# Optimization experiments

Hardware: AMD Instinct MI355X
Metric: run time of the kernel (lower is better)

Reference implementation:

```python
import jax, jax.numpy as jnp
import numpy as np

B, T, C = 8, 2048, 512
H = 16
HS = C // H  # 32, must equal HEAD_SIZE
TM_DIM = 32   # TIME_MIX_EXTRA_DIM
TD_DIM = 64   # TIME_DECAY_EXTRA_DIM
LAYER_ID, N_LAYER = 5, 12


def setup_inputs() -> dict:
    key = jax.random.key(0)
    ks = jax.random.split(key, 16)
    r01 = LAYER_ID / (N_LAYER - 1)
    r1a0 = 1.0 - LAYER_ID / N_LAYER
    ddd = (jnp.arange(C, dtype=jnp.float32) / C)
    n = jnp.arange(C, dtype=jnp.float32)
    decay_speed = -6.0 + 5.0 * (n / (C - 1)) ** (0.7 + 1.3 * r01)
    zigzag = ((n + 1) % 3 - 1) * 0.1
    faaaa = (r01 * (1 - n / (C - 1)) + zigzag).reshape(H, HS)
    s = 1.0 / np.sqrt(C)
    return {
        "x": jax.random.normal(ks[0], (B, T, C), dtype=jnp.float32),
        "time_maa_x": 1.0 - ddd ** r1a0,
        "time_maa_w": 1.0 - ddd ** r1a0,
        "time_maa_k": 1.0 - ddd ** r1a0,
        "time_maa_v": 1.0 - (ddd ** r1a0 + 0.3 * r01),
        "time_maa_r": 1.0 - ddd ** (0.5 * r1a0),
        "time_maa_g": 1.0 - ddd ** (0.5 * r1a0),
        "time_maa_w1": jax.random.uniform(ks[1], (C, TM_DIM * 5), minval=-1e-4, maxval=1e-4),
        "time_maa_w2": jax.random.uniform(ks[2], (5, TM_DIM, C), minval=-1e-4, maxval=1e-4),
        "time_decay": decay_speed,
        "time_decay_w1": jax.random.uniform(ks[3], (C, TD_DIM), minval=-1e-4, maxval=1e-4),
        "time_decay_w2": jax.random.uniform(ks[4], (TD_DIM, C), minval=-1e-4, maxval=1e-4),
        "time_faaaa": faaaa,
        "Wr": jax.random.normal(ks[5], (C, C)) * s,
        "Wk": jax.random.normal(ks[6], (C, C)) * s,
        "Wv": jax.random.normal(ks[7], (C, C)) * s,
        "Wg": jax.random.normal(ks[8], (C, C)) * s,
        "Wo": jax.random.normal(ks[9], (C, C)) * s,
        "ln_w": jnp.ones((C,), dtype=jnp.float32),
        "ln_b": jnp.zeros((C,), dtype=jnp.float32),
    }


def _wkv6(r, k, v, w, u):
    # r,k,v,w: (B,T,C); u: (H,HS). Linear recurrence per (batch, head).
    rs = r.reshape(B, T, H, HS).transpose(1, 0, 2, 3)
    ks_ = k.reshape(B, T, H, HS).transpose(1, 0, 2, 3)
    vs = v.reshape(B, T, H, HS).transpose(1, 0, 2, 3)
    # decay = exp(-exp(w)) per channel (the kernel passes ew = -exp(w))
    ds = jnp.exp(-jnp.exp(w.astype(jnp.float32))).reshape(B, T, H, HS).transpose(1, 0, 2, 3)
    ub = u[None, :, :, None]  # (1,H,HS_key,1)

    def step(S, inp):  # S: (B,H,HS_key,HS_val)
        r_t, k_t, v_t, d_t = inp
        kv = jnp.einsum("bhj,bhi->bhji", k_t, v_t)
        y = jnp.einsum("bhj,bhji->bhi", r_t, S + ub * kv)
        S = d_t[..., None] * S + kv
        return S, y

    S0 = jnp.zeros((B, H, HS, HS), dtype=jnp.float32)
    _, ys = jax.lax.scan(step, S0, (rs, ks_, vs, ds))
    return ys.transpose(1, 0, 2, 3).reshape(B, T, C)


def reference(x, time_maa_x, time_maa_w, time_maa_k, time_maa_v, time_maa_r,
              time_maa_g, time_maa_w1, time_maa_w2, time_decay, time_decay_w1,
              time_decay_w2, time_faaaa, Wr, Wk, Wv, Wg, Wo, ln_w, ln_b):
    # time shift: x_{t-1}, zeros at t=0  (ZeroPad2d((0,0,1,-1)))
    xshift = jnp.concatenate([jnp.zeros_like(x[:, :1]), x[:, :-1]], axis=1)
    xx = xshift - x
    xxx = x + xx * time_maa_x
    mix = jnp.tanh(jnp.einsum("btc,cd->btd", xxx, time_maa_w1)).reshape(B, T, 5, TM_DIM)
    mix = jnp.einsum("btfd,fdc->fbtc", mix, time_maa_w2)  # (5,B,T,C)
    mw, mk, mv, mr, mg = mix[0], mix[1], mix[2], mix[3], mix[4]
    xw = x + xx * (time_maa_w + mw)
    xk = x + xx * (time_maa_k + mk)
    xv = x + xx * (time_maa_v + mv)
    xr = x + xx * (time_maa_r + mr)
    xg = x + xx * (time_maa_g + mg)
    r = xr @ Wr.T
    k = xk @ Wk.T
    v = xv @ Wv.T
    g = jax.nn.silu(xg @ Wg.T)
    w = time_decay + jnp.tanh(xw @ time_decay_w1) @ time_decay_w2
    y = _wkv6(r, k, v, w, time_faaaa)
    # GroupNorm with H groups over channel dim, eps=1e-5
    yg = y.reshape(B, T, H, HS)
    mu = yg.mean(-1, keepdims=True)
    var = yg.var(-1, keepdims=True)
    yn = ((yg - mu) * jax.lax.rsqrt(var + 1e-5)).reshape(B, T, C)
    yn = yn * ln_w + ln_b
    return (yn * g) @ Wo.T
```

## Files before the change

kernel.cpp:

```cpp
#include <hip/hip_runtime.h>
#include <hip/hip_bf16.h>

#define B_ 8
#define T_ 2048
#define C_ 512
#define H_ 16
#define HS_ 32
#define BT_ (B_*T_)
#define CL_ 64
#define NC_ (T_/CL_)
#define STF_ 1056
#define WSZ_ 262144

typedef __hip_bfloat16 bf16;
typedef __attribute__((ext_vector_type(8))) short short8;
typedef __attribute__((ext_vector_type(4))) float f32x4;

__device__ __forceinline__ float b2f(bf16 v) { return __bfloat162float(v); }
__device__ __forceinline__ bf16 f2b(float v) { return __float2bfloat16(v); }

__global__ __launch_bounds__(256) void prep_combo_kernel(
    const float* __restrict__ x, const float* __restrict__ tmx,
    const float* __restrict__ Wr, const float* __restrict__ Wk,
    const float* __restrict__ Wv, const float* __restrict__ Wg,
    const float* __restrict__ Wo, const float* __restrict__ w1,
    const float* __restrict__ wd1, const float* __restrict__ w2,
    bf16* __restrict__ xxx, bf16* __restrict__ Wrb, bf16* __restrict__ Wkb,
    bf16* __restrict__ Wvb, bf16* __restrict__ Wgb, bf16* __restrict__ Wob,
    bf16* __restrict__ w1p, bf16* __restrict__ wd1p, bf16* __restrict__ w2p) {
  int idx = blockIdx.x * 256 + threadIdx.x;
  if (idx < BT_ * C_) {
    int c = idx & (C_ - 1);
    int t = (idx >> 9) & (T_ - 1);
    float xc = x[idx];
    float xp = (t == 0) ? 0.f : x[idx - C_];
    xxx[idx] = f2b(xc + (xp - xc) * tmx[c]);
    return;
  }
  idx -= BT_ * C_;
  if (idx < 5 * WSZ_) {
    int w = idx >> 18;
    int i = idx & (WSZ_ - 1);
    const float* src = (w == 0) ? Wr : (w == 1) ? Wk : (w == 2) ? Wv
                     : (w == 3) ? Wg : Wo;
    bf16* dst = (w == 0) ? Wrb : (w == 1) ? Wkb : (w == 2) ? Wvb
              : (w == 3) ? Wgb : Wob;
    float s = src[i];
    bf16 hi = f2b(s);
    dst[i] = hi;
    dst[WSZ_ + i] = f2b(s - b2f(hi));
    return;
  }
  idx -= 5 * WSZ_;
  if (idx < 192 * 512) {
    int n = idx >> 9, k = idx & (C_ - 1);
    w1p[idx] = f2b(n < 160 ? w1[k * 160 + n] : 0.f);
    return;
  }
  idx -= 192 * 512;
  if (idx < 64 * 512) {
    int n = idx >> 9, k = idx & (C_ - 1);
    wd1p[idx] = f2b(wd1[k * 64 + n]);
    return;
  }
  idx -= 64 * 512;
  {
    int c = idx / 192, n = idx - c * 192;
    w2p[idx] = f2b(n < 160 ? w2[(size_t)n * C_ + c] : 0.f);
  }
}
#define PREP_N_ ((BT_*C_ + 5*WSZ_ + 192*512 + 64*512 + 512*192) / 256)

template<int BN, int MODE, int SPLIT>
__global__ __launch_bounds__(256) void mfma_gemm_kernel(
    const bf16* __restrict__ A, const bf16* __restrict__ Bw,
    void* __restrict__ O, int N) {
  constexpr int BM = 128, BK = 32;
  constexpr int AE = BM * BK / 8;
  constexpr int BE = BN * BK / 8;
  __shared__ short8 Asm[AE];
  __shared__ short8 Bsm[BE];
  __shared__ short8 Lsm[SPLIT ? BE : 1];
  const int tid = threadIdx.x;
  const int lane = tid & 63;
  const int wave = tid >> 6;
  const int m0 = blockIdx.x * BM;
  const int n0 = blockIdx.y * BN;
  const int wm = (BN == 128) ? (wave >> 1) * 64 : wave * 32;
  const int wn = (BN == 128) ? (wave & 1) * 64 : 0;
  constexpr int MT = (BN == 128) ? 4 : 2;
  constexpr int NT = 4;
  f32x4 acc[MT][NT] = {};
  const int e0 = tid, e1 = tid + 256;
  const int r0 = ((e0 >> 6) << 4) | (e0 & 15), q0 = (e0 >> 4) & 3;
  const int r1 = ((e1 >> 6) << 4) | (e1 & 15), q1 = (e1 >> 4) & 3;
  const unsigned short* Au = (const unsigned short*)A;
  const unsigned short* Bu = (const unsigned short*)Bw;
  const unsigned short* Lu = Bu + (SPLIT ? WSZ_ : 0);
  for (int k0 = 0; k0 < C_; k0 += BK) {
    short8 a0 = *(const short8*)&Au[(size_t)(m0 + r0) * C_ + k0 + q0 * 8];
    short8 a1 = *(const short8*)&Au[(size_t)(m0 + r1) * C_ + k0 + q1 * 8];
    short8 b0 = *(const short8*)&Bu[(size_t)(n0 + r0) * C_ + k0 + q0 * 8];
    short8 b1, l0, l1;
    if constexpr (BN == 128)
      b1 = *(const short8*)&Bu[(size_t)(n0 + r1) * C_ + k0 + q1 * 8];
    if constexpr (SPLIT) {
      l0 = *(const short8*)&Lu[(size_t)(n0 + r0) * C_ + k0 + q0 * 8];
      if constexpr (BN == 128)
        l1 = *(const short8*)&Lu[(size_t)(n0 + r1) * C_ + k0 + q1 * 8];
    }
    __syncthreads();
    Asm[e0] = a0; Asm[e1] = a1;
    Bsm[e0] = b0;
    if constexpr (BN == 128) Bsm[e1] = b1;
    if constexpr (SPLIT) {
      Lsm[e0] = l0;
      if constexpr (BN == 128) Lsm[e1] = l1;
    }
    __syncthreads();
    short8 af[MT], bh[NT];
    #pragma unroll
    for (int mt = 0; mt < MT; ++mt) af[mt] = Asm[((wm >> 4) + mt) * 64 + lane];
    #pragma unroll
    for (int nt = 0; nt < NT; ++nt) bh[nt] = Bsm[((wn >> 4) + nt) * 64 + lane];
    #pragma unroll
    for (int mt = 0; mt < MT; ++mt)
      #pragma unroll
      for (int nt = 0; nt < NT; ++nt)
        acc[mt][nt] = __builtin_amdgcn_mfma_f32_16x16x32_bf16(
            af[mt], bh[nt], acc[mt][nt], 0, 0, 0);
    if constexpr (SPLIT) {
      short8 bl[NT];
      #pragma unroll
      for (int nt = 0; nt < NT; ++nt) bl[nt] = Lsm[((wn >> 4) + nt) * 64 + lane];
      #pragma unroll
      for (int mt = 0; mt < MT; ++mt)
        #pragma unroll
        for (int nt = 0; nt < NT; ++nt)
          acc[mt][nt] = __builtin_amdgcn_mfma_f32_16x16x32_bf16(
              af[mt], bl[nt], acc[mt][nt], 0, 0, 0);
    }
  }
  const int col = lane & 15, qr = lane >> 4;
  #pragma unroll
  for (int mt = 0; mt < MT; ++mt) {
    int mrow = m0 + wm + mt * 16 + qr * 4;
    #pragma unroll
    for (int nt = 0; nt < NT; ++nt) {
      int nc = n0 + wn + nt * 16 + col;
      #pragma unroll
      for (int r = 0; r < 4; ++r) {
        float v = acc[mt][nt][r];
        if (MODE == 1) v = v / (1.f + __expf(-v));
        if (MODE == 3) v = tanhf(v);
        size_t oi = (size_t)(mrow + r) * N + nc;
        if (MODE == 2) ((float*)O)[oi] = v;
        else           ((bf16*)O)[oi] = f2b(v);
      }
    }
  }
}

__global__ __launch_bounds__(256) void mix_mfma_kernel(
    const bf16* __restrict__ mix5, const bf16* __restrict__ w2p,
    const float* __restrict__ x,
    const float* __restrict__ tmw, const float* __restrict__ tmk,
    const float* __restrict__ tmv, const float* __restrict__ tmr,
    const float* __restrict__ tmg,
    bf16* __restrict__ xw, bf16* __restrict__ xk, bf16* __restrict__ xv,
    bf16* __restrict__ xr, bf16* __restrict__ xg) {
  constexpr int LDP = 200;
  __shared__ __align__(16) unsigned short Asm[64 * LDP];
  __shared__ __align__(16) unsigned short Bsm[64 * LDP];
  const int tid = threadIdx.x;
  const int row0 = blockIdx.x * 64;
  const int col0 = blockIdx.y * 64;
  const unsigned short* Au = (const unsigned short*)mix5;
  const unsigned short* Bu = (const unsigned short*)w2p;
  #pragma unroll
  for (int e0 = 0; e0 < 64 * 20; e0 += 256) {
    int e = e0 + tid;
    int rr = e / 20, p = e - rr * 20;
    *(short8*)&Asm[rr * LDP + p * 8] =
        *(const short8*)&Au[(size_t)(row0 + rr) * 192 + p * 8];
    *(short8*)&Bsm[rr * LDP + p * 8] =
        *(const short8*)&Bu[(size_t)(col0 + rr) * 192 + p * 8];
  }
  __syncthreads();
  const int lane = tid & 63, wave = tid >> 6;
  const int fl = lane & 15, q = lane >> 4;
  short8 af[5];
  #pragma unroll
  for (int f = 0; f < 5; ++f)
    af[f] = *(const short8*)&Asm[(wave * 16 + fl) * LDP + f * 32 + q * 8];
  f32x4 acc[4][5] = {};
  #pragma unroll
  for (int nt = 0; nt < 4; ++nt)
    #pragma unroll
    for (int f = 0; f < 5; ++f) {
      short8 bfr = *(const short8*)&Bsm[(nt * 16 + fl) * LDP + f * 32 + q * 8];
      acc[nt][f] = __builtin_amdgcn_mfma_f32_16x16x32_bf16(
          af[f], bfr, acc[nt][f], 0, 0, 0);
    }
  #pragma unroll
  for (int nt = 0; nt < 4; ++nt) {
    int cc = col0 + nt * 16 + fl;
    float vw = tmw[cc], vk = tmk[cc], vv = tmv[cc], vr = tmr[cc],
          vg = tmg[cc];
    #pragma unroll
    for (int r = 0; r < 4; ++r) {
      int rr = row0 + wave * 16 + q * 4 + r;
      size_t idx = (size_t)rr * C_ + cc;
      float xc = x[idx];
      float xx = (((rr & (T_ - 1)) == 0) ? 0.f : x[idx - C_]) - xc;
      xw[idx] = f2b(xc + xx * (vw + acc[nt][0][r]));
      xk[idx] = f2b(xc + xx * (vk + acc[nt][1][r]));
      xv[idx] = f2b(xc + xx * (vv + acc[nt][2][r]));
      xr[idx] = f2b(xc + xx * (vr + acc[nt][3][r]));
      xg[idx] = f2b(xc + xx * (vg + acc[nt][4][r]));
    }
  }
}

__global__ __launch_bounds__(512) void decay_kernel(
    const bf16* __restrict__ h1, const float* __restrict__ wd2,
    const float* __restrict__ tdecay, bf16* __restrict__ ee) {
  __shared__ float Hs[8][64];
  int row0 = blockIdx.x * 8;
  {
    int e = threadIdx.x;
    Hs[e >> 6][e & 63] = b2f(h1[(size_t)(row0 + (e >> 6)) * 64 + (e & 63)]);
  }
  __syncthreads();
  int c = threadIdx.x;
  float acc[8] = {0.f,0.f,0.f,0.f,0.f,0.f,0.f,0.f};
  for (int j = 0; j < 64; ++j) {
    float wv = wd2[j * C_ + c];
    #pragma unroll
    for (int r = 0; r < 8; ++r) acc[r] += Hs[r][j] * wv;
  }
  float td = tdecay[c];
  #pragma unroll
  for (int r = 0; r < 8; ++r)
    ee[(size_t)(row0 + r) * C_ + c] = f2b(expf(td + acc[r]));
}

__global__ __launch_bounds__(256) void wkv_partial_mfma(
    const bf16* __restrict__ k, const bf16* __restrict__ v,
    const bf16* __restrict__ ee, float* __restrict__ st) {
  __shared__ __align__(16) char smem[17536];
  float* Lm  = (float*)smem;
  bf16*  K2T = (bf16*)(smem + 8320);
  bf16*  VT  = (bf16*)(smem + 12928);
  bf16*  Eb  = K2T;
  int g = blockIdx.x;
  int bh = g >> 5, c = g & (NC_ - 1);
  int b = bh >> 4, h = bh & 15;
  const int tid = threadIdx.x;
  const int lane = tid & 63, wave = tid >> 6;
  const int ch = lane & 31, th = lane >> 5;
  size_t gbase = (size_t)b * T_ * C_ + (size_t)(c * CL_) * C_ + h * HS_;
  #pragma unroll
  for (int it = 0; it < 8; ++it) {
    int e = it * 256 + tid;
    Eb[e] = ee[gbase + (size_t)(e >> 5) * C_ + (e & 31)];
  }
  float kv[8]; bf16 vv[8];
  #pragma unroll
  for (int it = 0; it < 8; ++it) {
    int t = wave * 16 + it * 2 + th;
    size_t gi = gbase + (size_t)t * C_ + ch;
    kv[it] = b2f(k[gi]);
    vv[it] = v[gi];
  }
  __syncthreads();
  if (tid < 32) {
    float L = 0.f;
    for (int t = 0; t < CL_; ++t) {
      Lm[t * 32 + tid] = L;
      L -= b2f(Eb[t * 32 + tid]);
    }
    Lm[64 * 32 + tid] = L;
  }
  __syncthreads();
  float Ltot = Lm[64 * 32 + ch];
  #pragma unroll
  for (int it = 0; it < 8; ++it) {
    int t = wave * 16 + it * 2 + th;
    float Lt1 = Lm[(t + 1) * 32 + ch];
    K2T[ch * 72 + t] = f2b(kv[it] * __expf(Ltot - Lt1));
    VT [ch * 72 + t] = vv[it];
  }
  __syncthreads();
  const int fl = lane & 15, q = lane >> 4;
  const int mt = wave >> 1, nt = wave & 1;
  f32x4 accS = {};
  #pragma unroll
  for (int kc = 0; kc < 2; ++kc) {
    short8 av = *(const short8*)(VT + (mt * 16 + fl) * 72 + kc * 32 + q * 8);
    short8 bk = *(const short8*)(K2T + (nt * 16 + fl) * 72 + kc * 32 + q * 8);
    accS = __builtin_amdgcn_mfma_f32_16x16x32_bf16(av, bk, accS, 0, 0, 0);
  }
  size_t sbase = (size_t)g * STF_;
  #pragma unroll
  for (int r = 0; r < 4; ++r)
    st[sbase + (size_t)(mt * 16 + q * 4 + r) * 32 + nt * 16 + fl] = accS[r];
  if (tid < 32) st[sbase + 1024 + tid] = __expf(Lm[64 * 32 + tid]);
}

__global__ __launch_bounds__(64) void wkv_stitch_kernel(float* __restrict__ st) {
  int bh = blockIdx.x;
  int lane = threadIdx.x;
  int i = lane & 31, half = lane >> 5;
  float R[16];
  #pragma unroll
  for (int jj = 0; jj < 16; ++jj) R[jj] = 0.f;
  for (int c = 0; c < NC_; ++c) {
    size_t s = ((size_t)bh * NC_ + c) * STF_;
    float* sp = st + s + i * 32 + (half << 4);
    float Sc[16];
    float4* sc4 = reinterpret_cast<float4*>(Sc);
    float4* sp4 = reinterpret_cast<float4*>(sp);
    #pragma unroll
    for (int q = 0; q < 4; ++q) sc4[q] = sp4[q];
    float Pj[16];
    #pragma unroll
    for (int jj = 0; jj < 16; ++jj) Pj[jj] = st[s + 1024 + (half << 4) + jj];
    float4* r4 = reinterpret_cast<float4*>(R);
    #pragma unroll
    for (int q = 0; q < 4; ++q) sp4[q] = r4[q];
    #pragma unroll
    for (int jj = 0; jj < 16; ++jj) R[jj] = fmaf(Pj[jj], R[jj], Sc[jj]);
  }
}

__global__ __launch_bounds__(256) void wkv_final_mfma(
    const bf16* __restrict__ r, const bf16* __restrict__ k,
    const bf16* __restrict__ v, const bf16* __restrict__ ee,
    const float* __restrict__ faaaa, const float* __restrict__ st,
    const bf16* __restrict__ gg, const float* __restrict__ lnw,
    const float* __restrict__ lnb, bf16* __restrict__ z) {
  __shared__ __align__(16) char smem[29440];
  float* Lm = (float*)smem;
  bf16*  Pm = (bf16*)smem;
  bf16*  RA = (bf16*)(smem + 9216);
  bf16*  Kd = (bf16*)(smem + 14336);
  bf16*  VT = (bf16*)(smem + 19456);
  bf16*  Eb = VT;
  bf16*  Sh = (bf16*)(smem + 24064);
  bf16*  Sl = (bf16*)(smem + 26624);
  float* bon = (float*)(smem + 29184);
  int g = blockIdx.x;
  int bh = g >> 5, c = g & (NC_ - 1);
  int b = bh >> 4, h = bh & 15;
  const int tid = threadIdx.x;
  const int lane = tid & 63, wave = tid >> 6;
  const int ch = lane & 31, th = lane >> 5;
  size_t gbase = (size_t)b * T_ * C_ + (size_t)(c * CL_) * C_ + h * HS_;
  size_t sbase = (size_t)g * STF_;
  #pragma unroll
  for (int it = 0; it < 8; ++it) {
    int e = it * 256 + tid;
    Eb[e] = ee[gbase + (size_t)(e >> 5) * C_ + (e & 31)];
  }
  #pragma unroll
  for (int it = 0; it < 4; ++it) {
    int idx = it * 256 + tid;
    int i = idx >> 5, j = idx & 31;
    float s = st[sbase + idx];
    bf16 hi = f2b(s);
    Sh[i * 40 + j] = hi;
    Sl[i * 40 + j] = f2b(s - b2f(hi));
  }
  float rv[8], kv[8]; bf16 vv[8];
  #pragma unroll
  for (int it = 0; it < 8; ++it) {
    int t = wave * 16 + it * 2 + th;
    size_t gi = gbase + (size_t)t * C_ + ch;
    rv[it] = b2f(r[gi]); kv[it] = b2f(k[gi]); vv[it] = v[gi];
  }
  __syncthreads();
  if (tid < 32) {
    float L = 0.f;
    for (int t = 0; t < CL_; ++t) {
      Lm[t * 32 + tid] = L;
      L -= b2f(Eb[t * 32 + tid]);
    }
    Lm[64 * 32 + tid] = L;
  }
  __syncthreads();
  float u_j = faaaa[h * HS_ + ch];
  #pragma unroll
  for (int it = 0; it < 8; ++it) {
    int t = wave * 16 + it * 2 + th;
    float Lt  = Lm[t * 32 + ch];
    float Lt1 = Lm[(t + 1) * 32 + ch];
    RA[t * 40 + ch] = f2b(rv[it] * __expf(Lt));
    Kd[t * 40 + ch] = f2b(kv[it] * __expf(-Lt1));
    VT[ch * 72 + t] = vv[it];
    float pb = rv[it] * u_j * kv[it];
    pb += __shfl_xor(pb, 1); pb += __shfl_xor(pb, 2);
    pb += __shfl_xor(pb, 4); pb += __shfl_xor(pb, 8);
    pb += __shfl_xor(pb, 16);
    if (ch == 0) bon[t] = pb;
  }
  __syncthreads();
  const int fl = lane & 15, q = lane >> 4;
  short8 afr = *(const short8*)(RA + (wave * 16 + fl) * 40 + q * 8);
  f32x4 accY[2] = {};
  #pragma unroll
  for (int nt = 0; nt < 2; ++nt) {
    short8 sh = *(const short8*)(Sh + (nt * 16 + fl) * 40 + q * 8);
    short8 sl = *(const short8*)(Sl + (nt * 16 + fl) * 40 + q * 8);
    accY[nt] = __builtin_amdgcn_mfma_f32_16x16x32_bf16(afr, sh, accY[nt], 0, 0, 0);
    accY[nt] = __builtin_amdgcn_mfma_f32_16x16x32_bf16(afr, sl, accY[nt], 0, 0, 0);
  }
  f32x4 accP[4] = {};
  #pragma unroll
  for (int s4 = 0; s4 < 4; ++s4) {
    short8 bk = *(const short8*)(Kd + (s4 * 16 + fl) * 40 + q * 8);
    accP[s4] = __builtin_amdgcn_mfma_f32_16x16x32_bf16(afr, bk, accP[s4], 0, 0, 0);
  }
  #pragma unroll
  for (int s4 = 0; s4 < 4; ++s4)
    #pragma unroll
    for (int rr = 0; rr < 4; ++rr) {
      int t = wave * 16 + q * 4 + rr;
      int s = s4 * 16 + fl;
      float pv = accP[s4][rr];
      float bv = bon[t];
      pv = (s < t) ? pv : ((s == t) ? bv : 0.f);
      Pm[t * 72 + s] = f2b(pv);
    }
  __syncthreads();
  #pragma unroll
  for (int kc = 0; kc < 2; ++kc) {
    short8 ap = *(const short8*)(Pm + (wave * 16 + fl) * 72 + kc * 32 + q * 8);
    #pragma unroll
    for (int nt = 0; nt < 2; ++nt) {
      short8 bv = *(const short8*)(VT + (nt * 16 + fl) * 72 + kc * 32 + q * 8);
      accY[nt] = __builtin_amdgcn_mfma_f32_16x16x32_bf16(ap, bv, accY[nt], 0, 0, 0);
    }
  }
  float lw0 = lnw[h * HS_ + fl],      lb0 = lnb[h * HS_ + fl];
  float lw1 = lnw[h * HS_ + 16 + fl], lb1 = lnb[h * HS_ + 16 + fl];
  #pragma unroll
  for (int rr = 0; rr < 4; ++rr) {
    int t = wave * 16 + q * 4 + rr;
    float a0 = accY[0][rr], a1 = accY[1][rr];
    float mu = a0 + a1;
    mu += __shfl_xor(mu, 1); mu += __shfl_xor(mu, 2);
    mu += __shfl_xor(mu, 4); mu += __shfl_xor(mu, 8);
    mu *= (1.f / 32.f);
    float d0 = a0 - mu, d1 = a1 - mu;
    float ss = d0 * d0 + d1 * d1;
    ss += __shfl_xor(ss, 1); ss += __shfl_xor(ss, 2);
    ss += __shfl_xor(ss, 4); ss += __shfl_xor(ss, 8);
    float rs = rsqrtf(ss * (1.f / 32.f) + 1e-5f);
    size_t gi = gbase + (size_t)t * C_;
    float g0 = b2f(gg[gi + fl]);
    float g1 = b2f(gg[gi + 16 + fl]);
    z[gi + fl]      = f2b((d0 * rs * lw0 + lb0) * g0);
    z[gi + 16 + fl] = f2b((d1 * rs * lw1 + lb1) * g1);
  }
}

extern "C" void kernel_launch(void* const* d_in, const int* in_sizes, int n_in,
                              void* d_out, int out_size, void* d_ws, size_t ws_size,
                              hipStream_t stream) {
  (void)in_sizes; (void)n_in; (void)out_size; (void)ws_size;
  const float* x      = (const float*)d_in[0];
  const float* tmx    = (const float*)d_in[1];
  const float* tmw    = (const float*)d_in[2];
  const float* tmk    = (const float*)d_in[3];
  const float* tmv    = (const float*)d_in[4];
  const float* tmr    = (const float*)d_in[5];
  const float* tmg    = (const float*)d_in[6];
  const float* w1     = (const float*)d_in[7];
  const float* w2     = (const float*)d_in[8];
  const float* tdecay = (const float*)d_in[9];
  const float* wd1    = (const float*)d_in[10];
  const float* wd2    = (const float*)d_in[11];
  const float* faaaa  = (const float*)d_in[12];
  const float* Wr     = (const float*)d_in[13];
  const float* Wk     = (const float*)d_in[14];
  const float* Wv     = (const float*)d_in[15];
  const float* Wg     = (const float*)d_in[16];
  const float* Wo     = (const float*)d_in[17];
  const float* lnw    = (const float*)d_in[18];
  const float* lnb    = (const float*)d_in[19];
  float* out = (float*)d_out;

  char* w8 = (char*)d_ws;
  const size_t MB = 1024ull * 1024ull;
  bf16* S0 = (bf16*)(w8 +  0 * MB);
  bf16* S1 = (bf16*)(w8 + 16 * MB);
  bf16* S2 = (bf16*)(w8 + 32 * MB);
  bf16* S3 = (bf16*)(w8 + 48 * MB);
  bf16* S4 = (bf16*)(w8 + 64 * MB);
  bf16* S5 = (bf16*)(w8 + 80 * MB);
  float* st = (float*)(w8 + 96 * MB);
  char* wreg = w8 + 112 * MB + 512 * 1024;
  bf16* Wrb  = (bf16*)(wreg);
  bf16* Wkb  = Wrb + 2 * WSZ_;
  bf16* Wvb  = Wkb + 2 * WSZ_;
  bf16* Wgb  = Wvb + 2 * WSZ_;
  bf16* Wob  = Wgb + 2 * WSZ_;
  bf16* w1p  = Wob + 2 * WSZ_;
  bf16* wd1p = w1p + 192 * 512;
  bf16* w2p  = wd1p + 64 * 512;
  bf16* mix5p = S5;
  bf16* h1    = S5 + (size_t)BT_ * 192;

  prep_combo_kernel<<<PREP_N_, 256, 0, stream>>>(
      x, tmx, Wr, Wk, Wv, Wg, Wo, w1, wd1, w2,
      S0, Wrb, Wkb, Wvb, Wgb, Wob, w1p, wd1p, w2p);
  mfma_gemm_kernel<64, 3, 0><<<dim3(128, 3), 256, 0, stream>>>(S0, w1p, mix5p, 192);
  mix_mfma_kernel<<<dim3(BT_ / 64, 8), 256, 0, stream>>>(
      mix5p, w2p, x, tmw, tmk, tmv, tmr, tmg, S0, S1, S2, S3, S4);
  mfma_gemm_kernel<64, 3, 0><<<dim3(128, 1), 256, 0, stream>>>(S0, wd1p, h1, 64);
  decay_kernel<<<BT_ / 8, 512, 0, stream>>>(h1, wd2, tdecay, S0);
  dim3 gg(128, 4);
  mfma_gemm_kernel<128, 0, 1><<<gg, 256, 0, stream>>>(S3, Wrb, S5, C_);
  mfma_gemm_kernel<128, 0, 1><<<gg, 256, 0, stream>>>(S1, Wkb, S3, C_);
  mfma_gemm_kernel<128, 0, 1><<<gg, 256, 0, stream>>>(S2, Wvb, S1, C_);
  mfma_gemm_kernel<128, 1, 1><<<gg, 256, 0, stream>>>(S4, Wgb, S2, C_);
  wkv_partial_mfma<<<B_ * H_ * NC_, 256, 0, stream>>>(S3, S1, S0, st);
  wkv_stitch_kernel<<<B_ * H_, 64, 0, stream>>>(st);
  wkv_final_mfma<<<B_ * H_ * NC_, 256, 0, stream>>>(S5, S3, S1, S0, faaaa, st,
                                                    S2, lnw, lnb, S4);
  mfma_gemm_kernel<128, 2, 1><<<gg, 256, 0, stream>>>(S4, Wob, out, C_);
}
```

Before: 446.7 us.

## Load GEMM tiles directly into LDS and pre-split stitched state to bf16

```diff
diff --git a/kernel.cpp b/kernel.cpp
--- a/kernel.cpp
+++ b/kernel.cpp
@@ -18,6 +18,12 @@
 
 __device__ __forceinline__ float b2f(bf16 v) { return __bfloat162float(v); }
 __device__ __forceinline__ bf16 f2b(float v) { return __float2bfloat16(v); }
+
+__device__ __forceinline__ void gl2lds(const void* g, void* l) {
+  __builtin_amdgcn_global_load_lds(
+      (const __attribute__((address_space(1))) void*)g,
+      (__attribute__((address_space(3))) void*)l, 16, 0, 0);
+}
 
 __global__ __launch_bounds__(256) void prep_combo_kernel(
     const float* __restrict__ x, const float* __restrict__ tmx,
@@ -98,24 +104,16 @@
   const unsigned short* Bu = (const unsigned short*)Bw;
   const unsigned short* Lu = Bu + (SPLIT ? WSZ_ : 0);
   for (int k0 = 0; k0 < C_; k0 += BK) {
-    short8 a0 = *(const short8*)&Au[(size_t)(m0 + r0) * C_ + k0 + q0 * 8];
-    short8 a1 = *(const short8*)&Au[(size_t)(m0 + r1) * C_ + k0 + q1 * 8];
-    short8 b0 = *(const short8*)&Bu[(size_t)(n0 + r0) * C_ + k0 + q0 * 8];
-    short8 b1, l0, l1;
+    __syncthreads();
+    gl2lds(&Au[(size_t)(m0 + r0) * C_ + k0 + q0 * 8], &Asm[e0]);
+    gl2lds(&Au[(size_t)(m0 + r1) * C_ + k0 + q1 * 8], &Asm[e1]);
+    gl2lds(&Bu[(size_t)(n0 + r0) * C_ + k0 + q0 * 8], &Bsm[e0]);
     if constexpr (BN == 128)
-      b1 = *(const short8*)&Bu[(size_t)(n0 + r1) * C_ + k0 + q1 * 8];
+      gl2lds(&Bu[(size_t)(n0 + r1) * C_ + k0 + q1 * 8], &Bsm[e1]);
     if constexpr (SPLIT) {
-      l0 = *(const short8*)&Lu[(size_t)(n0 + r0) * C_ + k0 + q0 * 8];
+      gl2lds(&Lu[(size_t)(n0 + r0) * C_ + k0 + q0 * 8], &Lsm[e0]);
       if constexpr (BN == 128)
-        l1 = *(const short8*)&Lu[(size_t)(n0 + r1) * C_ + k0 + q1 * 8];
-    }
-    __syncthreads();
-    Asm[e0] = a0; Asm[e1] = a1;
-    Bsm[e0] = b0;
-    if constexpr (BN == 128) Bsm[e1] = b1;
-    if constexpr (SPLIT) {
-      Lsm[e0] = l0;
-      if constexpr (BN == 128) Lsm[e1] = l1;
+        gl2lds(&Lu[(size_t)(n0 + r1) * C_ + k0 + q1 * 8], &Lsm[e1]);
     }
     __syncthreads();
     short8 af[MT], bh[NT];
@@ -317,18 +315,31 @@
   for (int jj = 0; jj < 16; ++jj) R[jj] = 0.f;
   for (int c = 0; c < NC_; ++c) {
     size_t s = ((size_t)bh * NC_ + c) * STF_;
-    float* sp = st + s + i * 32 + (half << 4);
+    const float* sp = st + s + i * 32 + (half << 4);
     float Sc[16];
     float4* sc4 = reinterpret_cast<float4*>(Sc);
-    float4* sp4 = reinterpret_cast<float4*>(sp);
+    const float4* sp4 = reinterpret_cast<const float4*>(sp);
     #pragma unroll
     for (int q = 0; q < 4; ++q) sc4[q] = sp4[q];
     float Pj[16];
     #pragma unroll
     for (int jj = 0; jj < 16; ++jj) Pj[jj] = st[s + 1024 + (half << 4) + jj];
-    float4* r4 = reinterpret_cast<float4*>(R);
-    #pragma unroll
-    for (int q = 0; q < 4; ++q) sp4[q] = r4[q];
+    if (c > 0) {
+      __align__(16) bf16 hi16[16], lo16[16];
+      #pragma unroll
+      for (int jj = 0; jj < 16; ++jj) {
+        bf16 hb = f2b(R[jj]);
+        hi16[jj] = hb;
+        lo16[jj] = f2b(R[jj] - b2f(hb));
+      }
+      bf16* sb = (bf16*)(st + s - STF_);
+      short8* dh = (short8*)(sb + i * 32 + (half << 4));
+      short8* dl = (short8*)(sb + 1024 + i * 32 + (half << 4));
+      const short8* ph = (const short8*)hi16;
+      const short8* pl = (const short8*)lo16;
+      dh[0] = ph[0]; dh[1] = ph[1];
+      dl[0] = pl[0]; dl[1] = pl[1];
+    }
     #pragma unroll
     for (int jj = 0; jj < 16; ++jj) R[jj] = fmaf(Pj[jj], R[jj], Sc[jj]);
   }
@@ -340,22 +351,21 @@
     const float* __restrict__ faaaa, const float* __restrict__ st,
     const bf16* __restrict__ gg, const float* __restrict__ lnw,
     const float* __restrict__ lnb, bf16* __restrict__ z) {
-  __shared__ __align__(16) char smem[29440];
+  __shared__ __align__(16) char smem[24320];
   float* Lm = (float*)smem;
   bf16*  Pm = (bf16*)smem;
   bf16*  RA = (bf16*)(smem + 9216);
   bf16*  Kd = (bf16*)(smem + 14336);
   bf16*  VT = (bf16*)(smem + 19456);
   bf16*  Eb = VT;
-  bf16*  Sh = (bf16*)(smem + 24064);
-  bf16*  Sl = (bf16*)(smem + 26624);
-  float* bon = (float*)(smem + 29184);
+  float* bon = (float*)(smem + 24064);
   int g = blockIdx.x;
   int bh = g >> 5, c = g & (NC_ - 1);
   int b = bh >> 4, h = bh & 15;
   const int tid = threadIdx.x;
   const int lane = tid & 63, wave = tid >> 6;
   const int ch = lane & 31, th = lane >> 5;
+  const int fl = lane & 15, q = lane >> 4;
   size_t gbase = (size_t)b * T_ * C_ + (size_t)(c * CL_) * C_ + h * HS_;
   size_t sbase = (size_t)g * STF_;
   #pragma unroll
@@ -363,14 +373,14 @@
     int e = it * 256 + tid;
     Eb[e] = ee[gbase + (size_t)(e >> 5) * C_ + (e & 31)];
   }
-  #pragma unroll
-  for (int it = 0; it < 4; ++it) {
-    int idx = it * 256 + tid;
-    int i = idx >> 5, j = idx & 31;
-    float s = st[sbase + idx];
-    bf16 hi = f2b(s);
-    Sh[i * 40 + j] = hi;
-    Sl[i * 40 + j] = f2b(s - b2f(hi));
+  short8 sh[2] = {}, sl[2] = {};
+  if (c != 0) {
+    const unsigned short* sb = (const unsigned short*)(st + sbase - STF_);
+    #pragma unroll
+    for (int nt = 0; nt < 2; ++nt) {
+      sh[nt] = *(const short8*)&sb[(nt * 16 + fl) * 32 + q * 8];
+      sl[nt] = *(const short8*)&sb[1024 + (nt * 16 + fl) * 32 + q * 8];
+    }
   }
   float rv[8], kv[8]; bf16 vv[8];
   #pragma unroll
@@ -405,15 +415,12 @@
     if (ch == 0) bon[t] = pb;
   }
   __syncthreads();
-  const int fl = lane & 15, q = lane >> 4;
   short8 afr = *(const short8*)(RA + (wave * 16 + fl) * 40 + q * 8);
   f32x4 accY[2] = {};
   #pragma unroll
   for (int nt = 0; nt < 2; ++nt) {
-    short8 sh = *(const short8*)(Sh + (nt * 16 + fl) * 40 + q * 8);
-    short8 sl = *(const short8*)(Sl + (nt * 16 + fl) * 40 + q * 8);
-    accY[nt] = __builtin_amdgcn_mfma_f32_16x16x32_bf16(afr, sh, accY[nt], 0, 0, 0);
-    accY[nt] = __builtin_amdgcn_mfma_f32_16x16x32_bf16(afr, sl, accY[nt], 0, 0, 0);
+    accY[nt] = __builtin_amdgcn_mfma_f32_16x16x32_bf16(afr, sh[nt], accY[nt], 0, 0, 0);
+    accY[nt] = __builtin_amdgcn_mfma_f32_16x16x32_bf16(afr, sl[nt], accY[nt], 0, 0, 0);
   }
   f32x4 accP[4] = {};
   #pragma unroll
```

Result: faster. 431.2 us (-3.5%).
